# Performance work log

Measured on AMD Instinct MI355X. Metric: run time of the kernel, lower is better.

## Reference

```python
import jax, jax.numpy as jnp
import numpy as np

N, E, ND, ED, H, L = 50000, 800000, 64, 32, 128, 4
MIN = 2 * H + H + 1  # message MLP input dim = 385
EPS = 1e-5


def _layernorm(x, w, b):
    mu = x.mean(-1, keepdims=True)
    var = ((x - mu) ** 2).mean(-1, keepdims=True)
    return (x - mu) / jnp.sqrt(var + EPS) * w + b


def setup_inputs() -> dict:
    key = jax.random.key(0)
    ks = jax.random.split(key, 40)

    def w(k, shape):
        return jax.random.normal(k, shape, jnp.float32) / np.sqrt(shape[-2]).astype(np.float32)

    inp = {
        "node_features": jax.random.normal(ks[0], (N, ND), jnp.float32),
        "edge_features": jax.random.normal(ks[1], (E, ED), jnp.float32),
        "congestion": jax.random.uniform(ks[2], (N,), jnp.float32),
        "edge_index": jax.random.randint(ks[3], (2, E), 0, N),
        "unrouted_mask": jax.random.randint(ks[4], (N,), 0, 2).astype(jnp.bool_),
        "enc_node_w": w(ks[5], (ND, H)), "enc_node_b": jnp.zeros(H),
        "enc_edge_w": w(ks[6], (ED, H)), "enc_edge_b": jnp.zeros(H),
        "msg_w1": w(ks[7], (L, MIN, H)), "msg_b1": jnp.zeros((L, H)),
        "msg_w2": w(ks[8], (L, H, H)), "msg_b2": jnp.zeros((L, H)),
        "upd_w1": w(ks[9], (L, 2 * H, H)), "upd_b1": jnp.zeros((L, H)),
        "upd_w2": w(ks[10], (L, H, H)), "upd_b2": jnp.zeros((L, H)),
        "ln_w": jnp.ones((L, H)), "ln_b": jnp.zeros((L, H)),
        "unr_w1": w(ks[11], (1, H)), "unr_b1": jnp.zeros(H),
        "unr_w2": w(ks[12], (H, H)), "unr_b2": jnp.zeros(H),
        "ro_w1": w(ks[13], (2 * H, H)), "ro_b1": jnp.zeros(H),
        "ro_w2": w(ks[14], (H, H // 2)), "ro_b2": jnp.zeros(H // 2),
        "ro_w3": w(ks[15], (H // 2, 1)), "ro_b3": jnp.zeros(1),
    }
    return inp


def reference(node_features, edge_features, congestion, edge_index, unrouted_mask,
              enc_node_w, enc_node_b, enc_edge_w, enc_edge_b,
              msg_w1, msg_b1, msg_w2, msg_b2,
              upd_w1, upd_b1, upd_w2, upd_b2,
              ln_w, ln_b,
              unr_w1, unr_b1, unr_w2, unr_b2,
              ro_w1, ro_b1, ro_w2, ro_b2, ro_w3, ro_b3):
    n = node_features.shape[0]
    src, dst = edge_index[0], edge_index[1]

    x = node_features @ enc_node_w + enc_node_b            # [N, H]
    ea = edge_features @ enc_edge_w + enc_edge_b           # [E, H]
    cong_src = congestion[src][:, None]                    # [E, 1]

    for l in range(msg_w1.shape[0]):
        # message: gather src/dst features, concat with edge attr + congestion
        m_in = jnp.concatenate([x[src], x[dst], ea, cong_src], axis=-1)  # [E, 385]
        m = jax.nn.relu(m_in @ msg_w1[l] + msg_b1[l]) @ msg_w2[l] + msg_b2[l]  # [E, H]
        agg = jax.ops.segment_sum(m, dst, num_segments=n)  # scatter_add over dst
        u_in = jnp.concatenate([x, agg], axis=-1)          # [N, 2H]
        x_new = jax.nn.relu(u_in @ upd_w1[l] + upd_b1[l]) @ upd_w2[l] + upd_b2[l]
        x = _layernorm(x + x_new, ln_w[l], ln_b[l])        # dropout = identity (eval)

    graph_embed = x.mean(axis=0, keepdims=True)            # [1, H] (batch=None branch)
    unrouted_frac = unrouted_mask.astype(jnp.float32).mean()[None, None]  # [1, 1]
    unr = jax.nn.relu(unrouted_frac @ unr_w1 + unr_b1) @ unr_w2 + unr_b2  # [1, H]
    combined = jnp.concatenate([graph_embed, unr], axis=-1)  # [1, 2H]
    h = jax.nn.relu(combined @ ro_w1 + ro_b1)
    h = jax.nn.relu(h @ ro_w2 + ro_b2)
    out = jax.nn.sigmoid(h @ ro_w3 + ro_b3)                # [1, 1]
    return out.squeeze(-1)                                 # [1]
```

## Files before the change

kernel.cpp:

```cpp
#include <hip/hip_runtime.h>
#include <hip/hip_fp16.h>
#include <math.h>

#define NN 50000
#define EE 800000

typedef _Float16 half8 __attribute__((ext_vector_type(8)));
typedef float floatx4 __attribute__((ext_vector_type(4)));

__global__ void fold_kernel(const float* __restrict__ ew, const float* __restrict__ eb,
                            const float* __restrict__ w1, const float* __restrict__ b1,
                            float* __restrict__ Wc, float* __restrict__ b1f) {
  int l = blockIdx.y, c = blockIdx.x, j = threadIdx.x;
  __shared__ float row[128];
  const float* w1l = w1 + (size_t)l * 385 * 128;
  if (c < 32) {
    row[j] = ew[c * 128 + j];
    __syncthreads();
    float acc = 0.f;
    for (int k = 0; k < 128; k++) acc += row[k] * w1l[(256 + k) * 128 + j];
    Wc[((size_t)l * 32 + c) * 128 + j] = acc;
  } else {
    row[j] = eb[j];
    __syncthreads();
    float acc = b1[l * 128 + j];
    for (int k = 0; k < 128; k++) acc += row[k] * w1l[(256 + k) * 128 + j];
    b1f[l * 128 + j] = acc;
  }
}

__global__ void prep_w(const float* __restrict__ src, _Float16* __restrict__ dst,
                       int K, int perm) {
  int l = blockIdx.y;
  int lane = threadIdx.x;
  int kc = blockIdx.x >> 3, nt = blockIdx.x & 7;
  int n = nt * 16 + (lane & 15);
  int k0 = kc * 32 + (lane >> 4) * 8;
  const float* s = src + (size_t)l * K * 128;
  _Float16 out[8];
  for (int j = 0; j < 8; j++) {
    int k = k0 + j;
    int ks = perm ? ((k & 7) * 16 + (k >> 3)) : k;
    out[j] = (_Float16)s[(size_t)ks * 128 + n];
  }
  _Float16* d = dst + (((size_t)l * gridDim.x + blockIdx.x) * 64 + lane) * 8;
  *(half8*)d = *(half8*)out;
}

__global__ void prep_cong(const float* __restrict__ mw1, _Float16* __restrict__ w1cp) {
  int l = blockIdx.x, p = threadIdx.x;
  int col = (p & 7) * 16 + (p >> 3);
  w1cp[l * 128 + p] = (_Float16)mw1[((size_t)l * 385 + 384) * 128 + col];
}

__global__ void hist_kernel(const int* __restrict__ dstv, int* __restrict__ counts) {
  int e = blockIdx.x * 256 + threadIdx.x;
  if (e < EE) atomicAdd(&counts[dstv[e]], 1);
}

__global__ void scan1_kernel(const int* __restrict__ counts, int* __restrict__ offs,
                             int* __restrict__ bsum) {
  __shared__ int ws[16];
  int t = threadIdx.x, lane = t & 63, w = t >> 6;
  int i = blockIdx.x * 1024 + t;
  int v = (i < NN) ? counts[i] : 0;
  int s = v;
  for (int off = 1; off < 64; off <<= 1) {
    int u = __shfl_up(s, off);
    if (lane >= off) s += u;
  }
  if (lane == 63) ws[w] = s;
  __syncthreads();
  if (w == 0) {
    int u = (lane < 16) ? ws[lane] : 0;
    for (int off = 1; off < 16; off <<= 1) {
      int x = __shfl_up(u, off);
      if (lane >= off && lane < 16) u += x;
    }
    if (lane < 16) ws[lane] = u;
  }
  __syncthreads();
  int wbase = (w > 0) ? ws[w - 1] : 0;
  if (i < NN) offs[i] = wbase + s - v;
  if (t == 0) bsum[blockIdx.x] = ws[15];
}

__global__ void scan2_kernel(int* __restrict__ bsum) {
  int t = threadIdx.x;
  int v = (t < 49) ? bsum[t] : 0;
  int s = v;
  for (int off = 1; off < 64; off <<= 1) {
    int u = __shfl_up(s, off);
    if (t >= off) s += u;
  }
  if (t < 49) bsum[t] = s - v;
}

__global__ void slot1_kernel(const int* __restrict__ dstv, const int* __restrict__ offs,
                             const int* __restrict__ bsum, int* __restrict__ cursor,
                             int* __restrict__ einv) {
  int e = blockIdx.x * 256 + threadIdx.x;
  if (e >= EE) return;
  int d = dstv[e];
  int p = offs[d] + bsum[d >> 10] + atomicAdd(&cursor[d], 1);
  einv[p] = e;
}

__global__ void slot2_kernel(const int* __restrict__ einv, const int* __restrict__ srcv,
                             const int* __restrict__ dstv, const float* __restrict__ ef,
                             int2* __restrict__ meta, _Float16* __restrict__ efh) {
  int p = blockIdx.x * 256 + threadIdx.x;
  if (p >= EE) return;
  int e = einv[p];
  int2 m;
  m.x = srcv[e];
  m.y = dstv[e];
  meta[p] = m;
  const float* sp = ef + (size_t)e * 32;
  _Float16* dp = efh + (size_t)p * 32;
  for (int i = 0; i < 4; i++) {
    float4 f = *(const float4*)(sp + i * 8);
    float4 g = *(const float4*)(sp + i * 8 + 4);
    half8 v;
    v[0] = (_Float16)f.x; v[1] = (_Float16)f.y; v[2] = (_Float16)f.z; v[3] = (_Float16)f.w;
    v[4] = (_Float16)g.x; v[5] = (_Float16)g.y; v[6] = (_Float16)g.z; v[7] = (_Float16)g.w;
    *(half8*)(dp + i * 8) = v;
  }
}

__global__ void enc_mfma(const float* __restrict__ nf, const _Float16* __restrict__ Wenc,
                         const float* __restrict__ bn, _Float16* __restrict__ xh) {
  int t = threadIdx.x, wave = t >> 6, lane = t & 63;
  int quad = lane >> 4, l15 = lane & 15;
  long nb0 = (long)blockIdx.x * 64 + wave * 16;
  long rn = nb0 + l15;
  if (rn >= NN) rn = NN - 1;

  floatx4 acc[8] = {};
  for (int kc = 0; kc < 2; kc++) {
    const float* p = nf + rn * 64 + kc * 32 + quad * 8;
    float4 f0 = *(const float4*)p;
    float4 f1 = *(const float4*)(p + 4);
    half8 a;
    a[0] = (_Float16)f0.x; a[1] = (_Float16)f0.y;
    a[2] = (_Float16)f0.z; a[3] = (_Float16)f0.w;
    a[4] = (_Float16)f1.x; a[5] = (_Float16)f1.y;
    a[6] = (_Float16)f1.z; a[7] = (_Float16)f1.w;
    const _Float16* bp = Wenc + (size_t)(kc * 8) * 512 + lane * 8;
    for (int nt = 0; nt < 8; nt++) {
      half8 b = *(const half8*)(bp + nt * 512);
      acc[nt] = __builtin_amdgcn_mfma_f32_16x16x32_f16(a, b, acc[nt], 0, 0, 0);
    }
  }
  float bv[8];
  for (int nt = 0; nt < 8; nt++) bv[nt] = bn[nt * 16 + l15];
  for (int reg = 0; reg < 4; reg++) {
    long n = nb0 + quad * 4 + reg;
    if (n < NN) {
      for (int nt = 0; nt < 8; nt++)
        xh[n * 128 + nt * 16 + l15] = (_Float16)(acc[nt][reg] + bv[nt]);
    }
  }
}

__global__ __launch_bounds__(256, 3) void sd_kernel(
    const _Float16* __restrict__ xh, const _Float16* __restrict__ WSa,
    const _Float16* __restrict__ WSb, const float* __restrict__ b1f,
    _Float16* __restrict__ Sh, _Float16* __restrict__ Dh) {
  int t = threadIdx.x, wave = t >> 6, lane = t & 63;
  int quad = lane >> 4, l15 = lane & 15;
  long nb0 = (long)blockIdx.x * 64 + wave * 16;
  long rn = nb0 + l15;
  if (rn >= NN) rn = NN - 1;

  floatx4 as_[8] = {}, ad[8] = {};
#pragma unroll
  for (int kc = 0; kc < 4; kc++) {
    half8 a = *(const half8*)(xh + rn * 128 + kc * 32 + quad * 8);
    const _Float16* bpa = WSa + (size_t)(kc * 8) * 512 + lane * 8;
    const _Float16* bpb = WSb + (size_t)(kc * 8) * 512 + lane * 8;
#pragma unroll
    for (int nt = 0; nt < 8; nt++) {
      half8 ba = *(const half8*)(bpa + nt * 512);
      half8 bb = *(const half8*)(bpb + nt * 512);
      as_[nt] = __builtin_amdgcn_mfma_f32_16x16x32_f16(a, ba, as_[nt], 0, 0, 0);
      ad[nt] = __builtin_amdgcn_mfma_f32_16x16x32_f16(a, bb, ad[nt], 0, 0, 0);
    }
  }
  float bbv[8];
  for (int nt = 0; nt < 8; nt++) bbv[nt] = b1f[nt * 16 + l15];
  for (int reg = 0; reg < 4; reg++) {
    long n = nb0 + quad * 4 + reg;
    if (n < NN) {
      half8 hs, hd;
      for (int nt = 0; nt < 8; nt++) {
        hs[nt] = (_Float16)as_[nt][reg];
        hd[nt] = (_Float16)(ad[nt][reg] + bbv[nt]);
      }
      *(half8*)(Sh + n * 128 + l15 * 8) = hs;
      *(half8*)(Dh + n * 128 + l15 * 8) = hd;
    }
  }
}

__global__ __launch_bounds__(256, 4) void msg_kernel(
    const _Float16* __restrict__ Sh, const _Float16* __restrict__ Dh,
    const _Float16* __restrict__ efh, const int2* __restrict__ meta,
    const float* __restrict__ cong,
    const _Float16* __restrict__ Wcp, const _Float16* __restrict__ Wp2,
    const _Float16* __restrict__ w1cp, const float* __restrict__ b2,
    __half* __restrict__ agg) {
  __shared__ __align__(16) _Float16 As[128][136];
  __shared__ int s_src[128], s_dst[128];
  __shared__ float s_cg[128];
  int t = threadIdx.x, wave = t >> 6, lane = t & 63;
  int quad = lane >> 4, l15 = lane & 15;
  long eb0 = (long)blockIdx.x * 128;
  int web = wave * 32;
  if (t < 128) {
    int2 m = meta[eb0 + t];
    s_src[t] = m.x;
    s_dst[t] = m.y;
    s_cg[t] = cong[m.x];
  }
  __syncthreads();

  half8 wcl = *(const half8*)(w1cp + l15 * 8);

#pragma unroll
  for (int mtl = 0; mtl < 2; mtl++) {
    int rbase = web + mtl * 16;
    half8 sv[4], dv[4];
#pragma unroll
    for (int reg = 0; reg < 4; reg++) {
      int r = rbase + quad * 4 + reg;
      sv[reg] = *(const half8*)(Sh + (size_t)s_src[r] * 128 + l15 * 8);
      dv[reg] = *(const half8*)(Dh + (size_t)s_dst[r] * 128 + l15 * 8);
    }
    half8 a = *(const half8*)(efh + (size_t)(eb0 + rbase + l15) * 32 + quad * 8);
    floatx4 e[8] = {};
#pragma unroll
    for (int nt = 0; nt < 8; nt++) {
      half8 b = *(const half8*)(Wcp + (size_t)nt * 512 + lane * 8);
      e[nt] = __builtin_amdgcn_mfma_f32_16x16x32_f16(a, b, e[nt], 0, 0, 0);
    }
#pragma unroll
    for (int reg = 0; reg < 4; reg++) {
      int r = rbase + quad * 4 + reg;
      float cg = s_cg[r];
      half8 hv;
#pragma unroll
      for (int nt = 0; nt < 8; nt++) {
        float v = (float)sv[reg][nt] + (float)dv[reg][nt] + e[nt][reg] +
                  cg * (float)wcl[nt];
        hv[nt] = (_Float16)fmaxf(v, 0.f);
      }
      *(half8*)&As[r][l15 * 8] = hv;
    }
  }
  __syncthreads();

  int nb = wave * 2;
  floatx4 acc2[8][2] = {};
#pragma unroll
  for (int kc = 0; kc < 4; kc++) {
    const _Float16* bp = Wp2 + ((size_t)(kc * 8 + nb)) * 512 + lane * 8;
    half8 b0 = *(const half8*)bp;
    half8 b1v = *(const half8*)(bp + 512);
#pragma unroll
    for (int mt = 0; mt < 8; mt++) {
      half8 a = *(const half8*)&As[mt * 16 + l15][kc * 32 + quad * 8];
      acc2[mt][0] = __builtin_amdgcn_mfma_f32_16x16x32_f16(a, b0, acc2[mt][0], 0, 0, 0);
      acc2[mt][1] = __builtin_amdgcn_mfma_f32_16x16x32_f16(a, b1v, acc2[mt][1], 0, 0, 0);
    }
  }
  __syncthreads();

  {
    float c0 = b2[nb * 16 + l15], c1 = b2[(nb + 1) * 16 + l15];
#pragma unroll
    for (int mt = 0; mt < 8; mt++)
#pragma unroll
      for (int reg = 0; reg < 4; reg++) {
        int row = mt * 16 + quad * 4 + reg;
#pragma unroll
        for (int ntp = 0; ntp < 2; ntp++) {
          float v = acc2[mt][ntp][reg] + (ntp ? c1 : c0);
          float p = __shfl_xor(v, 1);
          if ((l15 & 1) == 0) {
            __half2 h = __halves2half2(__float2half(v), __float2half(p));
            *(__half2*)&As[row][(nb + ntp) * 16 + l15] = h;
          }
        }
      }
  }
  __syncthreads();

  {
    int cp = t & 63;
    int q = t >> 6;
    int r0 = q * 32;
    __half2 vals[32];
#pragma unroll
    for (int i = 0; i < 32; i++) vals[i] = *(__half2*)&As[r0 + i][cp * 2];
    int cur = s_dst[r0];
    float a0 = 0.f, a1 = 0.f;
    for (int i = 0; i < 32; i++) {
      int d = s_dst[r0 + i];
      if (d != cur) {
        unsafeAtomicAdd((__half2*)(agg + (long)cur * 128 + cp * 2),
                        __halves2half2(__float2half(a0), __float2half(a1)));
        a0 = a1 = 0.f;
        cur = d;
      }
      float2 f = __half22float2(vals[i]);
      a0 += f.x;
      a1 += f.y;
    }
    unsafeAtomicAdd((__half2*)(agg + (long)cur * 128 + cp * 2),
                    __halves2half2(__float2half(a0), __float2half(a1)));
  }
}

__global__ __launch_bounds__(256, 3) void upd_kernel(
    _Float16* __restrict__ xh, const _Float16* __restrict__ agg,
    const _Float16* __restrict__ Wp1, const _Float16* __restrict__ Wp2,
    const float* __restrict__ b1, const float* __restrict__ b2,
    const float* __restrict__ g, const float* __restrict__ bb) {
  __shared__ __align__(16) _Float16 hs[4][16][136];
  int t = threadIdx.x, wave = t >> 6, lane = t & 63;
  int quad = lane >> 4, l15 = lane & 15;
  long nb0 = (long)blockIdx.x * 64 + wave * 16;

  floatx4 acc[8] = {};
  {
    long n = nb0 + l15;
    long rn = n < NN ? n : NN - 1;
    for (int kc = 0; kc < 8; kc++) {
      half8 a;
      if (kc < 4) {
        a = *(const half8*)(xh + rn * 128 + kc * 32 + quad * 8);
      } else {
        a = *(const half8*)(agg + rn * 128 + (kc - 4) * 32 + quad * 8);
      }
      const _Float16* bp = Wp1 + (size_t)(kc * 8) * 512 + lane * 8;
      for (int nt = 0; nt < 8; nt++) {
        half8 b = *(const half8*)(bp + nt * 512);
        acc[nt] = __builtin_amdgcn_mfma_f32_16x16x32_f16(a, b, acc[nt], 0, 0, 0);
      }
    }
  }

  float bbv[8];
  for (int nt = 0; nt < 8; nt++) bbv[nt] = b1[nt * 16 + l15];
  for (int reg = 0; reg < 4; reg++) {
    half8 hv;
    for (int nt = 0; nt < 8; nt++)
      hv[nt] = (_Float16)fmaxf(acc[nt][reg] + bbv[nt], 0.f);
    *(half8*)&hs[wave][quad * 4 + reg][l15 * 8] = hv;
  }
  __syncthreads();

  floatx4 acc2[8] = {};
  for (int kc = 0; kc < 4; kc++) {
    half8 a = *(const half8*)&hs[wave][l15][kc * 32 + quad * 8];
    const _Float16* bp = Wp2 + (size_t)(kc * 8) * 512 + lane * 8;
    for (int nt = 0; nt < 8; nt++) {
      half8 b = *(const half8*)(bp + nt * 512);
      acc2[nt] = __builtin_amdgcn_mfma_f32_16x16x32_f16(a, b, acc2[nt], 0, 0, 0);
    }
  }

  float b2v[8], gv[8], bv[8];
  for (int nt = 0; nt < 8; nt++) {
    int col = nt * 16 + l15;
    b2v[nt] = b2[col]; gv[nt] = g[col]; bv[nt] = bb[col];
  }
  for (int reg = 0; reg < 4; reg++) {
    long n = nb0 + quad * 4 + reg;
    bool ok = n < NN;
    long rn = ok ? n : NN - 1;
    float y[8];
    float s = 0.f;
    for (int nt = 0; nt < 8; nt++) {
      y[nt] = (float)xh[rn * 128 + nt * 16 + l15] + acc2[nt][reg] + b2v[nt];
      s += y[nt];
    }
    s += __shfl_xor(s, 1); s += __shfl_xor(s, 2);
    s += __shfl_xor(s, 4); s += __shfl_xor(s, 8);
    float mu = s * (1.f / 128.f);
    float q = 0.f;
    for (int nt = 0; nt < 8; nt++) {
      y[nt] -= mu;
      q += y[nt] * y[nt];
    }
    q += __shfl_xor(q, 1); q += __shfl_xor(q, 2);
    q += __shfl_xor(q, 4); q += __shfl_xor(q, 8);
    float rstd = rsqrtf(q * (1.f / 128.f) + 1e-5f);
    if (ok) {
      for (int nt = 0; nt < 8; nt++) {
        float o = y[nt] * rstd * gv[nt] + bv[nt];
        xh[n * 128 + nt * 16 + l15] = (_Float16)o;
      }
    }
  }
}

__global__ void reduce_kernel(const _Float16* __restrict__ xh,
                              const int* __restrict__ umask, float* __restrict__ red) {
  int t = threadIdx.x;
  long base = (long)blockIdx.x * 196;
  int j = t & 127, half = t >> 7;
  float acc = 0.f;
  for (int i = 0; i < 98; i++) {
    long n = base + half + 2L * i;
    if (n < NN) acc += (float)xh[n * 128 + j];
  }
  __shared__ float sr[2][128];
  __shared__ float sm[4];
  sr[half][j] = acc;
  float mv = 0.f;
  {
    long n = base + t;
    if (t < 196 && n < NN) mv = (float)umask[n];
  }
  for (int off = 32; off; off >>= 1) mv += __shfl_xor(mv, off);
  if ((t & 63) == 0) sm[t >> 6] = mv;
  __syncthreads();
  if (t < 128) atomicAdd(&red[t], sr[0][t] + sr[1][t]);
  if (t == 0) atomicAdd(&red[128], sm[0] + sm[1] + sm[2] + sm[3]);
}

__global__ void readout_kernel(const float* __restrict__ red,
                               const float* __restrict__ xw1, const float* __restrict__ xb1,
                               const float* __restrict__ xw2, const float* __restrict__ xb2,
                               const float* __restrict__ rw1, const float* __restrict__ rb1,
                               const float* __restrict__ rw2, const float* __restrict__ rb2,
                               const float* __restrict__ rw3, const float* __restrict__ rb3,
                               float* __restrict__ out) {
  __shared__ float sa[128], sb[128], sc[128];
  int j = threadIdx.x;
  const float inv = 1.f / (float)NN;
  float ge = red[j] * inv;
  float uf = red[128] * inv;
  float u1 = fmaxf(uf * xw1[j] + xb1[j], 0.f);
  sa[j] = u1;
  sb[j] = ge;
  __syncthreads();
  float u2 = xb2[j];
  for (int k = 0; k < 128; k++) u2 += sa[k] * xw2[k * 128 + j];
  sc[j] = u2;
  __syncthreads();
  float h1 = rb1[j];
  for (int k = 0; k < 128; k++) h1 += sb[k] * rw1[k * 128 + j];
  for (int k = 0; k < 128; k++) h1 += sc[k] * rw1[(128 + k) * 128 + j];
  h1 = fmaxf(h1, 0.f);
  __syncthreads();
  sa[j] = h1;
  __syncthreads();
  float h2 = 0.f;
  if (j < 64) {
    h2 = rb2[j];
    for (int k = 0; k < 128; k++) h2 += sa[k] * rw2[k * 64 + j];
    h2 = fmaxf(h2, 0.f);
  }
  __syncthreads();
  if (j < 64) sb[j] = h2;
  __syncthreads();
  if (j == 0) {
    float a = rb3[0];
    for (int k = 0; k < 64; k++) a += sb[k] * rw3[k];
    out[0] = 1.f / (1.f + expf(-a));
  }
}

extern "C" void kernel_launch(void* const* d_in, const int* in_sizes, int n_in,
                              void* d_out, int out_size, void* d_ws, size_t ws_size,
                              hipStream_t stream) {
  const float* nf   = (const float*)d_in[0];
  const float* ef   = (const float*)d_in[1];
  const float* cong = (const float*)d_in[2];
  const int*   eidx = (const int*)d_in[3];
  const int*   um   = (const int*)d_in[4];
  const float* enw  = (const float*)d_in[5];
  const float* enb  = (const float*)d_in[6];
  const float* eew  = (const float*)d_in[7];
  const float* eeb  = (const float*)d_in[8];
  const float* mw1  = (const float*)d_in[9];
  const float* mb1  = (const float*)d_in[10];
  const float* mw2  = (const float*)d_in[11];
  const float* mb2  = (const float*)d_in[12];
  const float* uw1  = (const float*)d_in[13];
  const float* ub1  = (const float*)d_in[14];
  const float* uw2  = (const float*)d_in[15];
  const float* ub2  = (const float*)d_in[16];
  const float* lnw  = (const float*)d_in[17];
  const float* lnb  = (const float*)d_in[18];
  const float* xw1  = (const float*)d_in[19];
  const float* xb1  = (const float*)d_in[20];
  const float* xw2  = (const float*)d_in[21];
  const float* xb2  = (const float*)d_in[22];
  const float* rw1  = (const float*)d_in[23];
  const float* rb1  = (const float*)d_in[24];
  const float* rw2  = (const float*)d_in[25];
  const float* rb2  = (const float*)d_in[26];
  const float* rw3  = (const float*)d_in[27];
  const float* rb3  = (const float*)d_in[28];
  float* out = (float*)d_out;

  char* W = (char*)d_ws;
  _Float16* xh    = (_Float16*)(W + 0);
  __half*   agg   = (__half*)(W + 12800000);
  _Float16* efh   = (_Float16*)(W + 25600000);
  _Float16* Sh    = (_Float16*)(W + 76800000);
  _Float16* Dh    = (_Float16*)(W + 89600000);
  int2*     meta  = (int2*)(W + 102400000);
  int*      einv  = (int*)(W + 108800000);
  int*      counts= (int*)(W + 112000000);
  int*      cursor= (int*)(W + 112200000);
  int*      offs  = (int*)(W + 112400000);
  _Float16* WSa   = (_Float16*)(W + 112600000);
  _Float16* WSb   = (_Float16*)(W + 112731072);
  _Float16* Wcp   = (_Float16*)(W + 112862144);
  _Float16* Wm2   = (_Float16*)(W + 112894912);
  _Float16* Wu1   = (_Float16*)(W + 113025984);
  _Float16* Wu2   = (_Float16*)(W + 113288128);
  _Float16* Wen   = (_Float16*)(W + 113419200);
  float*    Wc    = (float*)(W + 113435584);
  float*    b1f   = (float*)(W + 113501120);
  _Float16* w1cp  = (_Float16*)(W + 113503168);
  float*    red   = (float*)(W + 113504192);
  int*      bsum  = (int*)red;

  const int* srcv = eidx;
  const int* dstv = eidx + EE;

  (void)hipMemsetAsync(counts, 0, 400000, stream);
  hist_kernel<<<3125, 256, 0, stream>>>(dstv, counts);
  scan1_kernel<<<49, 1024, 0, stream>>>(counts, offs, bsum);
  scan2_kernel<<<1, 64, 0, stream>>>(bsum);
  slot1_kernel<<<3125, 256, 0, stream>>>(dstv, offs, bsum, cursor, einv);
  slot2_kernel<<<3125, 256, 0, stream>>>(einv, srcv, dstv, ef, meta, efh);

  fold_kernel<<<dim3(33, 4), 128, 0, stream>>>(eew, eeb, mw1, mb1, Wc, b1f);
  prep_w<<<dim3(8, 4), 64, 0, stream>>>(Wc, Wcp, 32, 0);
  prep_w<<<dim3(32, 4), 64, 0, stream>>>(mw1, WSa, 385, 0);
  prep_w<<<dim3(32, 4), 64, 0, stream>>>(mw1 + 128 * 128, WSb, 385, 0);
  prep_w<<<dim3(32, 4), 64, 0, stream>>>(mw2, Wm2, 128, 1);
  prep_w<<<dim3(64, 4), 64, 0, stream>>>(uw1, Wu1, 256, 0);
  prep_w<<<dim3(32, 4), 64, 0, stream>>>(uw2, Wu2, 128, 1);
  prep_w<<<dim3(16, 1), 64, 0, stream>>>(enw, Wen, 64, 0);
  prep_cong<<<4, 128, 0, stream>>>(mw1, w1cp);
  enc_mfma<<<782, 256, 0, stream>>>(nf, Wen, enb, xh);

  for (int l = 0; l < 4; l++) {
    sd_kernel<<<782, 256, 0, stream>>>(
        xh, WSa + (size_t)l * 32 * 512, WSb + (size_t)l * 32 * 512,
        b1f + l * 128, Sh, Dh);
    (void)hipMemsetAsync(agg, 0, (size_t)NN * 128 * sizeof(__half), stream);
    msg_kernel<<<6250, 256, 0, stream>>>(
        Sh, Dh, efh, meta, cong,
        Wcp + (size_t)l * 8 * 512, Wm2 + (size_t)l * 32 * 512,
        w1cp + l * 128, mb2 + l * 128, agg);
    upd_kernel<<<782, 256, 0, stream>>>(
        xh, (const _Float16*)agg,
        Wu1 + (size_t)l * 64 * 512, Wu2 + (size_t)l * 32 * 512,
        ub1 + l * 128, ub2 + l * 128, lnw + l * 128, lnb + l * 128);
  }

  (void)hipMemsetAsync(red, 0, 129 * sizeof(float), stream);
  reduce_kernel<<<256, 256, 0, stream>>>(xh, um, red);
  readout_kernel<<<1, 128, 0, stream>>>(red, xw1, xb1, xw2, xb2,
                                        rw1, rb1, rw2, rb2, rw3, rb3, out);
}
```

Before: 931.5 us.

## Remap msg blocks across XCDs, hoist gathers, and use packed fp16 math

Remaps the message kernel's block index so consecutive edge tiles land on the same XCD, which aims to improve L2 locality for the sorted destination gathers. All src/dst row gathers and the edge-feature loads are now issued up front, before the first MFMA, to expose more memory-level parallelism, at the cost of more live registers. The first-layer epilogue and the segmented reduction now use packed fp16 arithmetic instead of fp32, and the shuffle-based half2 store is replaced with direct scalar LDS writes. MFMA priority is raised via s_setprio. Accumulating in fp16 lowers precision, and the extra registers may hurt occupancy.

```diff
diff --git a/kernel.cpp b/kernel.cpp
--- a/kernel.cpp
+++ b/kernel.cpp
@@ -6,6 +6,7 @@
 #define EE 800000
 
 typedef _Float16 half8 __attribute__((ext_vector_type(8)));
+typedef __fp16 fp16x2 __attribute__((ext_vector_type(2)));
 typedef float floatx4 __attribute__((ext_vector_type(4)));
 
 __global__ void fold_kernel(const float* __restrict__ ew, const float* __restrict__ eb,
@@ -215,29 +216,39 @@
   __shared__ float s_cg[128];
   int t = threadIdx.x, wave = t >> 6, lane = t & 63;
   int quad = lane >> 4, l15 = lane & 15;
-  long eb0 = (long)blockIdx.x * 128;
+
+  int orig = blockIdx.x, nwg = gridDim.x;
+  int qq = nwg >> 3, rr = nwg & 7;
+  int xcd = orig & 7, rk = orig >> 3;
+  int bb = (xcd < rr) ? (xcd * (qq + 1) + rk)
+                      : (rr * (qq + 1) + (xcd - rr) * qq + rk);
+  long eb0 = (long)bb * 128;
   int web = wave * 32;
+
   if (t < 128) {
     int2 m = meta[eb0 + t];
     s_src[t] = m.x;
     s_dst[t] = m.y;
     s_cg[t] = cong[m.x];
   }
-  __syncthreads();
-
   half8 wcl = *(const half8*)(w1cp + l15 * 8);
+  half8 av0 = *(const half8*)(efh + (size_t)(eb0 + web + l15) * 32 + quad * 8);
+  half8 av1 = *(const half8*)(efh + (size_t)(eb0 + web + 16 + l15) * 32 + quad * 8);
+  __syncthreads();
+
+  half8 sv[8], dv[8];
+#pragma unroll
+  for (int mtl = 0; mtl < 2; mtl++)
+#pragma unroll
+    for (int reg = 0; reg < 4; reg++) {
+      int r = web + mtl * 16 + quad * 4 + reg;
+      sv[mtl * 4 + reg] = *(const half8*)(Sh + (size_t)s_src[r] * 128 + l15 * 8);
+      dv[mtl * 4 + reg] = *(const half8*)(Dh + (size_t)s_dst[r] * 128 + l15 * 8);
+    }
 
 #pragma unroll
   for (int mtl = 0; mtl < 2; mtl++) {
-    int rbase = web + mtl * 16;
-    half8 sv[4], dv[4];
-#pragma unroll
-    for (int reg = 0; reg < 4; reg++) {
-      int r = rbase + quad * 4 + reg;
-      sv[reg] = *(const half8*)(Sh + (size_t)s_src[r] * 128 + l15 * 8);
-      dv[reg] = *(const half8*)(Dh + (size_t)s_dst[r] * 128 + l15 * 8);
-    }
-    half8 a = *(const half8*)(efh + (size_t)(eb0 + rbase + l15) * 32 + quad * 8);
+    half8 a = mtl ? av1 : av0;
     floatx4 e[8] = {};
 #pragma unroll
     for (int nt = 0; nt < 8; nt++) {
@@ -246,22 +257,28 @@
     }
 #pragma unroll
     for (int reg = 0; reg < 4; reg++) {
-      int r = rbase + quad * 4 + reg;
-      float cg = s_cg[r];
-      half8 hv;
-#pragma unroll
-      for (int nt = 0; nt < 8; nt++) {
-        float v = (float)sv[reg][nt] + (float)dv[reg][nt] + e[nt][reg] +
-                  cg * (float)wcl[nt];
-        hv[nt] = (_Float16)fmaxf(v, 0.f);
-      }
-      *(half8*)&As[r][l15 * 8] = hv;
+      int r = web + mtl * 16 + quad * 4 + reg;
+      _Float16 cgh = (_Float16)s_cg[r];
+      half8 v = sv[mtl * 4 + reg] + dv[mtl * 4 + reg];
+      half8 e8;
+#pragma unroll
+      for (int i = 0; i < 4; i++) {
+        fp16x2 p = __builtin_amdgcn_cvt_pkrtz(e[2 * i][reg], e[2 * i + 1][reg]);
+        e8[2 * i] = (_Float16)p[0];
+        e8[2 * i + 1] = (_Float16)p[1];
+      }
+      v += e8;
+      v += wcl * cgh;
+#pragma unroll
+      for (int i = 0; i < 8; i++) v[i] = v[i] > (_Float16)0 ? v[i] : (_Float16)0;
+      *(half8*)&As[r][l15 * 8] = v;
     }
   }
   __syncthreads();
 
   int nb = wave * 2;
   floatx4 acc2[8][2] = {};
+  __builtin_amdgcn_s_setprio(1);
 #pragma unroll
   for (int kc = 0; kc < 4; kc++) {
     const _Float16* bp = Wp2 + ((size_t)(kc * 8 + nb)) * 512 + lane * 8;
@@ -274,6 +291,7 @@
       acc2[mt][1] = __builtin_amdgcn_mfma_f32_16x16x32_f16(a, b1v, acc2[mt][1], 0, 0, 0);
     }
   }
+  __builtin_amdgcn_s_setprio(0);
   __syncthreads();
 
   {
@@ -283,42 +301,31 @@
 #pragma unroll
       for (int reg = 0; reg < 4; reg++) {
         int row = mt * 16 + quad * 4 + reg;
-#pragma unroll
-        for (int ntp = 0; ntp < 2; ntp++) {
-          float v = acc2[mt][ntp][reg] + (ntp ? c1 : c0);
-          float p = __shfl_xor(v, 1);
-          if ((l15 & 1) == 0) {
-            __half2 h = __halves2half2(__float2half(v), __float2half(p));
-            *(__half2*)&As[row][(nb + ntp) * 16 + l15] = h;
-          }
-        }
+        As[row][nb * 16 + l15] = (_Float16)(acc2[mt][0][reg] + c0);
+        As[row][(nb + 1) * 16 + l15] = (_Float16)(acc2[mt][1][reg] + c1);
       }
   }
   __syncthreads();
 
   {
     int cp = t & 63;
-    int q = t >> 6;
-    int r0 = q * 32;
+    int q8 = t >> 6;
+    int r0 = q8 * 32;
     __half2 vals[32];
 #pragma unroll
     for (int i = 0; i < 32; i++) vals[i] = *(__half2*)&As[r0 + i][cp * 2];
     int cur = s_dst[r0];
-    float a0 = 0.f, a1 = 0.f;
+    __half2 acc = __float2half2_rn(0.f);
     for (int i = 0; i < 32; i++) {
       int d = s_dst[r0 + i];
       if (d != cur) {
-        unsafeAtomicAdd((__half2*)(agg + (long)cur * 128 + cp * 2),
-                        __halves2half2(__float2half(a0), __float2half(a1)));
-        a0 = a1 = 0.f;
+        unsafeAtomicAdd((__half2*)(agg + (long)cur * 128 + cp * 2), acc);
+        acc = __float2half2_rn(0.f);
         cur = d;
       }
-      float2 f = __half22float2(vals[i]);
-      a0 += f.x;
-      a1 += f.y;
-    }
-    unsafeAtomicAdd((__half2*)(agg + (long)cur * 128 + cp * 2),
-                    __halves2half2(__float2half(a0), __float2half(a1)));
+      acc = __hadd2(acc, vals[i]);
+    }
+    unsafeAtomicAdd((__half2*)(agg + (long)cur * 128 + cp * 2), acc);
   }
 }
 
```

New measurement: 935.9 us. No clear change (+0.5%).
